# Kernel optimization log

Measured on AMD Instinct MI355X. Metric: run time of the kernel, lower is better.

The kernel has to match this reference:

```python
import jax, jax.numpy as jnp
import numpy as np
from jax import lax

K_STEEP = 10.0      # ssm_K: surrogate spike steepness
V_TH_MIN = 0.1      # ssm_v_th_min
EK_FLOOR = 0.01     # ssm_ek_floor


def setup_inputs() -> dict:
    key = jax.random.key(0)
    ks = jax.random.split(key, 11)
    B, T, D, N = 2, 1024, 1024, 16
    s = lambda fan: 1.0 / np.sqrt(fan)
    return {
        "hidden_states": jax.random.normal(ks[0], (B, T, D), jnp.float32),
        "W_xz": jax.random.normal(ks[1], (D, 2 * D), jnp.float32) * s(D),
        "W_dt": jax.random.normal(ks[2], (D, D), jnp.float32) * s(D),
        "b_dt": jax.random.normal(ks[3], (D,), jnp.float32) * 0.1,
        "A_log": jax.random.uniform(ks[4], (D, N), jnp.float32, 0.0, 1.0),
        "W_B": jax.random.normal(ks[5], (D, N), jnp.float32) * s(D),
        "W_C": jax.random.normal(ks[6], (D, N), jnp.float32) * s(D),
        "D_skip": jax.random.normal(ks[7], (D,), jnp.float32) * 0.1,
        "W_out": jax.random.normal(ks[8], (D, D), jnp.float32) * s(D),
        "v_th": jax.random.uniform(ks[9], (D,), jnp.float32, 0.0, 0.5),
    }


def _bio_ssm(h, W_xz, W_dt, b_dt, A_log, W_B, W_C, D_skip, W_out, v_th):
    # h: (T, B, D) time-major, as in the torch wrapper after permute(1,0,2)
    T, B, D = h.shape
    N = A_log.shape[1]
    xz = jnp.einsum('tbd,de->tbe', h, W_xz)
    x, z = jnp.split(xz, 2, axis=-1)                       # (T,B,D) each
    dt = jax.nn.softplus(jnp.einsum('tbd,de->tbe', x, W_dt) + b_dt)  # (T,B,D)
    A = -jnp.exp(A_log)                                     # (D,N), negative
    Bm = jnp.einsum('tbd,dn->tbn', h, W_B)                  # (T,B,N)
    Cm = jnp.einsum('tbd,dn->tbn', h, W_C)                  # (T,B,N)
    decay = jnp.exp(dt[..., None] * A)                      # (T,B,D,N)
    inp = (dt * x)[..., None] * Bm[:, :, None, :]           # (T,B,D,N)

    def step(s, td):
        dec, ip, c = td
        s = dec * s + ip                                    # (B,D,N)
        y = jnp.einsum('bdn,bn->bd', s, c)
        return s, y

    s0 = jnp.zeros((B, D, N), h.dtype)
    _, y = lax.scan(step, s0, (decay, inp, Cm))             # y: (T,B,D)
    y = y + D_skip * x
    vth = jnp.maximum(v_th, V_TH_MIN)
    spike_p = jax.nn.sigmoid(K_STEEP * (y - vth))           # surrogate spiking gate
    y_sp = y * spike_p
    pc = jnp.mean(spike_p)                                  # ponder cost
    efc = jnp.mean(jax.nn.relu(EK_FLOOR - y * y))           # ek-floor cost
    out = jnp.einsum('tbd,de->tbe', y_sp * jax.nn.silu(z), W_out)
    return out, pc, efc


def reference(hidden_states, W_xz, W_dt, b_dt, A_log, W_B, W_C, D_skip, W_out, v_th):
    h = jnp.transpose(hidden_states, (1, 0, 2))             # (T,B,D)
    h_out, pc, efc = _bio_ssm(h, W_xz, W_dt, b_dt, A_log, W_B, W_C, D_skip, W_out, v_th)
    out = h_out - h                                         # mixer residual delta
    return jnp.transpose(out, (1, 0, 2))                    # (B,T,D)
```

## Files before the change

kernel.cpp:

```cpp
#include <hip/hip_runtime.h>
#include <hip/hip_bf16.h>
#include <stdint.h>

#define TT 1024
#define BB 2
#define DD 1024
#define NN 16
#define NCH 64
#define LCH 16

#define K_STEEP 10.0f
#define V_TH_MIN 0.1f
#define L2E 1.44269504088896f

typedef __bf16 bf16x8 __attribute__((ext_vector_type(8)));
typedef float f32x4 __attribute__((ext_vector_type(4)));

__device__ __forceinline__ short f2bf(float f) {
    union { float f; unsigned u; } c; c.f = f;
    unsigned r = (c.u + 0x7fffu + ((c.u >> 16) & 1u)) >> 16;
    return (short)r;
}

__device__ __forceinline__ void gload_lds16(const void* g, void* l) {
    __builtin_amdgcn_global_load_lds(
        (const __attribute__((address_space(1))) void*)g,
        (__attribute__((address_space(3))) void*)l, 16, 0, 0);
}

template<int BM, int EPI, bool FUSE_BC>
__global__ __launch_bounds__(256) void gemm_mfma(
    const short* __restrict__ A,
    const short* __restrict__ BT,
    float* __restrict__ C, int ldc,
    int M, int Ncols, int K,
    const float* __restrict__ bias,
    const float* __restrict__ sub,
    short* __restrict__ xbuf,
    const short* __restrict__ WbcT,
    float* __restrict__ bcout)
{
    constexpr int RI = BM / 32;
    constexpr int AS_SZ = (FUSE_BC && BM * 32 < 2048) ? 2048 : BM * 32;
    __shared__ short As[AS_SZ];
    __shared__ short Bs[128 * 32];

    const int tid = threadIdx.x;
    const int wave = tid >> 6, lane = tid & 63;
    const int kk = (lane >> 4) * 8;
    const int r16 = lane & 15;
    const int wr = wave >> 1, wc = wave & 1;

    if (FUSE_BC && blockIdx.x == gridDim.x - 1) {
        const int bm2 = blockIdx.y * 32;
        f32x4 acc2 = {};
        for (int k0 = 0; k0 < K; k0 += 64) {
            int off = tid * 16;
            int row = off >> 7;
            int ke  = (off & 127) >> 1;
            gload_lds16(A + (size_t)(bm2 + row) * K + k0 + ke, (char*)As + off);
            gload_lds16(WbcT + (size_t)row * K + k0 + ke, (char*)Bs + off);
            __syncthreads();
            bf16x8 alo = *(const bf16x8*)&As[(wr * 16 + r16) * 64 + kk];
            bf16x8 ahi = *(const bf16x8*)&As[(wr * 16 + r16) * 64 + kk + 32];
            bf16x8 blo = *(const bf16x8*)&Bs[(wc * 16 + r16) * 64 + kk];
            bf16x8 bhi = *(const bf16x8*)&Bs[(wc * 16 + r16) * 64 + kk + 32];
            acc2 = __builtin_amdgcn_mfma_f32_16x16x32_bf16(alo, blo, acc2, 0, 0, 0);
            acc2 = __builtin_amdgcn_mfma_f32_16x16x32_bf16(ahi, bhi, acc2, 0, 0, 0);
            __syncthreads();
        }
        #pragma unroll
        for (int g = 0; g < 4; g++) {
            int row = bm2 + wr * 16 + (lane >> 4) * 4 + g;
            int col = wc * 16 + r16;
            bcout[(size_t)row * 32 + col] = acc2[g];
        }
        return;
    }

    const int bm = blockIdx.y * BM, bn = blockIdx.x * 128;
    f32x4 acc[RI][4] = {};

    for (int k0 = 0; k0 < K; k0 += 32) {
        #pragma unroll
        for (int it = 0; it < 2; it++) {
            int off = it * 4096 + tid * 16;
            int row = off >> 6;
            int ke  = (off & 63) >> 1;
            gload_lds16(BT + (size_t)(bn + row) * K + k0 + ke, (char*)Bs + off);
        }
        if (tid < BM * 4) {
            int off = tid * 16;
            int row = off >> 6;
            int ke  = (off & 63) >> 1;
            gload_lds16(A + (size_t)(bm + row) * K + k0 + ke, (char*)As + off);
        }
        __syncthreads();

        bf16x8 a[RI], b[4];
        #pragma unroll
        for (int i = 0; i < RI; i++)
            a[i] = *(const bf16x8*)&As[(wr * (BM / 2) + i * 16 + r16) * 32 + kk];
        #pragma unroll
        for (int j = 0; j < 4; j++)
            b[j] = *(const bf16x8*)&Bs[(wc * 64 + j * 16 + r16) * 32 + kk];
        #pragma unroll
        for (int i = 0; i < RI; i++)
            #pragma unroll
            for (int j = 0; j < 4; j++)
                acc[i][j] = __builtin_amdgcn_mfma_f32_16x16x32_bf16(
                    a[i], b[j], acc[i][j], 0, 0, 0);
        __syncthreads();
    }

    #pragma unroll
    for (int i = 0; i < RI; i++) {
        #pragma unroll
        for (int j = 0; j < 4; j++) {
            #pragma unroll
            for (int g = 0; g < 4; g++) {
                int row = bm + wr * (BM / 2) + i * 16 + (lane >> 4) * 4 + g;
                int col = bn + wc * 64 + j * 16 + r16;
                float v = acc[i][j][g];
                if (EPI == 1) {
                    v += bias[col];
                    v = fmaxf(v, 0.f) + log1pf(__expf(-fabsf(v)));
                }
                if (EPI == 2) {
                    v -= sub[(size_t)row * ldc + col];
                }
                C[(size_t)row * ldc + col] = v;
                if (EPI == 3 && col < DD) {
                    xbuf[(size_t)row * DD + col] = f2bf(v);
                }
            }
        }
    }
}

__device__ __forceinline__ void tr_tile(
    const float* __restrict__ W, short* __restrict__ WT,
    int K, int N, int k0, int n0, int tid)
{
    __shared__ float t[32][33];
    int r = tid >> 3, q = tid & 7;
    float4 v = *(const float4*)&W[(size_t)(k0 + r) * N + n0 + q * 4];
    t[r][q * 4 + 0] = v.x; t[r][q * 4 + 1] = v.y;
    t[r][q * 4 + 2] = v.z; t[r][q * 4 + 3] = v.w;
    __syncthreads();
    short4 o = { f2bf(t[q * 4 + 0][r]), f2bf(t[q * 4 + 1][r]),
                 f2bf(t[q * 4 + 2][r]), f2bf(t[q * 4 + 3][r]) };
    *(short4*)&WT[(size_t)(n0 + r) * K + k0 + q * 4] = o;
}

__global__ __launch_bounds__(256) void prep_all(
    const float* __restrict__ H,    short* __restrict__ Hb,
    const float* __restrict__ W_xz, short* __restrict__ WxzT,
    const float* __restrict__ W_dt, short* __restrict__ WdtT,
    const float* __restrict__ W_out,short* __restrict__ WoutT,
    const float* __restrict__ W_B,  const float* __restrict__ W_C,
    short* __restrict__ WbcT)
{
    int bid = blockIdx.x, tid = threadIdx.x;
    if (bid < 2048) {
        int i = bid * 1024 + tid * 4;
        float4 v = *(const float4*)&H[i];
        short4 o = { f2bf(v.x), f2bf(v.y), f2bf(v.z), f2bf(v.w) };
        *(short4*)&Hb[i] = o;
    } else if (bid < 4096) {
        int t = bid - 2048;
        tr_tile(W_xz, WxzT, DD, 2 * DD, (t >> 6) * 32, (t & 63) * 32, tid);
    } else if (bid < 5120) {
        int t = bid - 4096;
        tr_tile(W_dt, WdtT, DD, DD, (t >> 5) * 32, (t & 31) * 32, tid);
    } else if (bid < 6144) {
        int t = bid - 5120;
        tr_tile(W_out, WoutT, DD, DD, (t >> 5) * 32, (t & 31) * 32, tid);
    } else {
        int g = (bid - 6144) * 256 + tid;
        int k = g & (DD - 1);
        int n = g >> 10;
        float v = (n < 16) ? W_B[(size_t)k * NN + n]
                           : W_C[(size_t)k * NN + n - 16];
        WbcT[(size_t)n * DD + k] = f2bf(v);
    }
}

__global__ __launch_bounds__(256) void scan_phase1(
    const float* __restrict__ xz,
    const float* __restrict__ dtb,
    const float* __restrict__ bc,
    const float* __restrict__ A_log,
    float* __restrict__ Lst,
    float* __restrict__ sdt)
{
    int tid = threadIdx.x;
    int d = blockIdx.x * 256 + tid;
    int b = blockIdx.y;
    int c = blockIdx.z;

    __shared__ float sBm[LCH][NN];
    for (int i = tid; i < LCH * NN; i += 256) {
        int j = i >> 4, n = i & 15;
        int r = b * TT + c * LCH + j;
        sBm[j][n] = bc[(size_t)r * 32 + n];
    }
    __syncthreads();

    float a2[NN];
    #pragma unroll
    for (int n = 0; n < NN; n++)
        a2[n] = -__expf(A_log[(size_t)d * NN + n]) * L2E;

    float s[NN];
    #pragma unroll
    for (int n = 0; n < NN; n++) s[n] = 0.f;

    float sum_dt = 0.f;
    for (int j = 0; j < LCH; j++) {
        int r = b * TT + c * LCH + j;
        float dt = dtb[(size_t)r * DD + d];
        float x  = xz[(size_t)r * (2 * DD) + d];
        float dtx = dt * x;
        sum_dt += dt;
        #pragma unroll
        for (int n = 0; n < NN; n++) {
            float dec = exp2f(a2[n] * dt);
            s[n] = fmaf(dec, s[n], dtx * sBm[j][n]);
        }
    }
    size_t base = ((size_t)(c * BB + b) * DD + d) * NN;
    #pragma unroll
    for (int n = 0; n < NN; n++) Lst[base + n] = s[n];
    sdt[(size_t)(c * BB + b) * DD + d] = sum_dt;
}

__global__ __launch_bounds__(256) void scan_phase2(
    const float* __restrict__ A_log,
    const float* __restrict__ Lst,
    const float* __restrict__ sdt,
    float* __restrict__ Sinit)
{
    int g = blockIdx.x * 256 + threadIdx.x;
    int n = g & 15;
    int d = (g >> 4) & (DD - 1);
    int b = g >> 14;
    float a2 = -__expf(A_log[(size_t)d * NN + n]) * L2E;
    float s = 0.f;
    for (int c = 0; c < NCH; c++) {
        size_t idx = ((size_t)(c * BB + b) * DD + d) * NN + n;
        Sinit[idx] = s;
        float P = exp2f(a2 * sdt[(size_t)(c * BB + b) * DD + d]);
        s = fmaf(P, s, Lst[idx]);
    }
}

__global__ __launch_bounds__(256) void scan_phase3(
    const float* __restrict__ xz,
    const float* __restrict__ dtb,
    const float* __restrict__ bc,
    const float* __restrict__ A_log,
    const float* __restrict__ Sinit,
    const float* __restrict__ D_skip,
    const float* __restrict__ v_th,
    short* __restrict__ gout)
{
    int tid = threadIdx.x;
    int d = blockIdx.x * 256 + tid;
    int b = blockIdx.y;
    int c = blockIdx.z;

    __shared__ float sB[LCH][NN];
    __shared__ float sC[LCH][NN];
    for (int i = tid; i < LCH * 32; i += 256) {
        int j = i >> 5, m = i & 31;
        int r = b * TT + c * LCH + j;
        float v = bc[(size_t)r * 32 + m];
        if (m < 16) sB[j][m] = v; else sC[j][m - 16] = v;
    }
    __syncthreads();

    float a2[NN];
    #pragma unroll
    for (int n = 0; n < NN; n++)
        a2[n] = -__expf(A_log[(size_t)d * NN + n]) * L2E;

    size_t base = ((size_t)(c * BB + b) * DD + d) * NN;
    float s[NN];
    #pragma unroll
    for (int n = 0; n < NN; n++) s[n] = Sinit[base + n];

    float dsk = D_skip[d];
    float vth = fmaxf(v_th[d], V_TH_MIN);

    for (int j = 0; j < LCH; j++) {
        int r = b * TT + c * LCH + j;
        float dt = dtb[(size_t)r * DD + d];
        float x  = xz[(size_t)r * (2 * DD) + d];
        float z  = xz[(size_t)r * (2 * DD) + DD + d];
        float dtx = dt * x;
        float y = 0.f;
        #pragma unroll
        for (int n = 0; n < NN; n++) {
            float dec = exp2f(a2[n] * dt);
            s[n] = fmaf(dec, s[n], dtx * sB[j][n]);
            y = fmaf(s[n], sC[j][n], y);
        }
        y = fmaf(dsk, x, y);
        float sp = 1.f / (1.f + __expf(-K_STEEP * (y - vth)));
        float sz = z / (1.f + __expf(-z));
        gout[(size_t)r * DD + d] = f2bf(y * sp * sz);
    }
}

extern "C" void kernel_launch(void* const* d_in, const int* in_sizes, int n_in,
                              void* d_out, int out_size, void* d_ws, size_t ws_size,
                              hipStream_t stream) {
    const float* H      = (const float*)d_in[0];
    const float* W_xz   = (const float*)d_in[1];
    const float* W_dt   = (const float*)d_in[2];
    const float* b_dt   = (const float*)d_in[3];
    const float* A_log  = (const float*)d_in[4];
    const float* W_B    = (const float*)d_in[5];
    const float* W_C    = (const float*)d_in[6];
    const float* D_skip = (const float*)d_in[7];
    const float* W_out  = (const float*)d_in[8];
    const float* v_th   = (const float*)d_in[9];
    float* out = (float*)d_out;

    float* ws  = (float*)d_ws;
    float* xz  = ws;
    float* dtb = xz  + 4194304;
    float* bcb = dtb + 2097152;
    float* Lst = bcb + 65536;
    float* sdt = Lst + 2097152;
    float* Sin = sdt + 131072;
    short* p16   = (short*)(Sin + 2097152);
    short* Hb    = p16;
    short* WxzT  = Hb    + 2097152;
    short* WdtT  = WxzT  + 2097152;
    short* WoutT = WdtT  + 1048576;
    short* WbcT  = WoutT + 1048576;
    short* xb    = WbcT  + 32768;
    short* gb    = xb    + 2097152;

    const int M = BB * TT;

    prep_all<<<6272, 256, 0, stream>>>(
        H, Hb, W_xz, WxzT, W_dt, WdtT, W_out, WoutT, W_B, W_C, WbcT);
    gemm_mfma<32, 3, true><<<dim3(17, M / 32), 256, 0, stream>>>(
        Hb, WxzT, xz, 2 * DD, M, 2 * DD, DD, nullptr, nullptr, xb, WbcT, bcb);
    gemm_mfma<32, 1, false><<<dim3(8, M / 32), 256, 0, stream>>>(
        xb, WdtT, dtb, DD, M, DD, DD, b_dt, nullptr, nullptr, nullptr, nullptr);
    scan_phase1<<<dim3(DD / 256, BB, NCH), 256, 0, stream>>>(
        xz, dtb, bcb, A_log, Lst, sdt);
    scan_phase2<<<(BB * DD * NN) / 256, 256, 0, stream>>>(A_log, Lst, sdt, Sin);
    scan_phase3<<<dim3(DD / 256, BB, NCH), 256, 0, stream>>>(
        xz, dtb, bcb, A_log, Sin, D_skip, v_th, gb);
    gemm_mfma<32, 2, false><<<dim3(8, M / 32), 256, 0, stream>>>(
        gb, WoutT, out, DD, M, DD, DD, nullptr, H, nullptr, nullptr, nullptr);
}
```

Measured before the change: 126.7 us.

## Fuse three-phase chunked scan into one kernel and store xz as bf16

The three scan kernels (local chunk scan, cross-chunk carry propagation, final scan with gating) are merged into one kernel. Each block covers 8 channels across all 64 chunks and passes chunk states through shared memory, so the Lst/sdt/Sinit global round trips and two launches go away. The xz projection output is now written only as bf16 and read directly by the dt GEMM (via a new lda stride) and by the scan. This halves xz traffic and drops the separate x buffer, at the cost of lower precision for x and z in the scan. The new scan layout makes each thread read one d from a row, so dt and xz loads become less coalesced (8 contiguous channels per row).

```diff
diff --git a/kernel.cpp b/kernel.cpp
--- a/kernel.cpp
+++ b/kernel.cpp
@@ -21,6 +21,11 @@
     unsigned r = (c.u + 0x7fffu + ((c.u >> 16) & 1u)) >> 16;
     return (short)r;
 }
+__device__ __forceinline__ float bf2f(short s) {
+    union { unsigned u; float f; } c;
+    c.u = ((unsigned)(unsigned short)s) << 16;
+    return c.f;
+}
 
 __device__ __forceinline__ void gload_lds16(const void* g, void* l) {
     __builtin_amdgcn_global_load_lds(
@@ -30,13 +35,13 @@
 
 template<int BM, int EPI, bool FUSE_BC>
 __global__ __launch_bounds__(256) void gemm_mfma(
-    const short* __restrict__ A,
+    const short* __restrict__ A, int lda,
     const short* __restrict__ BT,
     float* __restrict__ C, int ldc,
     int M, int Ncols, int K,
     const float* __restrict__ bias,
     const float* __restrict__ sub,
-    short* __restrict__ xbuf,
+    short* __restrict__ bf16out,
     const short* __restrict__ WbcT,
     float* __restrict__ bcout)
 {
@@ -58,7 +63,7 @@
             int off = tid * 16;
             int row = off >> 7;
             int ke  = (off & 127) >> 1;
-            gload_lds16(A + (size_t)(bm2 + row) * K + k0 + ke, (char*)As + off);
+            gload_lds16(A + (size_t)(bm2 + row) * lda + k0 + ke, (char*)As + off);
             gload_lds16(WbcT + (size_t)row * K + k0 + ke, (char*)Bs + off);
             __syncthreads();
             bf16x8 alo = *(const bf16x8*)&As[(wr * 16 + r16) * 64 + kk];
@@ -93,7 +98,7 @@
             int off = tid * 16;
             int row = off >> 6;
             int ke  = (off & 63) >> 1;
-            gload_lds16(A + (size_t)(bm + row) * K + k0 + ke, (char*)As + off);
+            gload_lds16(A + (size_t)(bm + row) * lda + k0 + ke, (char*)As + off);
         }
         __syncthreads();
 
@@ -122,16 +127,17 @@
                 int row = bm + wr * (BM / 2) + i * 16 + (lane >> 4) * 4 + g;
                 int col = bn + wc * 64 + j * 16 + r16;
                 float v = acc[i][j][g];
-                if (EPI == 1) {
-                    v += bias[col];
-                    v = fmaxf(v, 0.f) + log1pf(__expf(-fabsf(v)));
-                }
-                if (EPI == 2) {
-                    v -= sub[(size_t)row * ldc + col];
-                }
-                C[(size_t)row * ldc + col] = v;
-                if (EPI == 3 && col < DD) {
-                    xbuf[(size_t)row * DD + col] = f2bf(v);
+                if (EPI == 3) {
+                    bf16out[(size_t)row * ldc + col] = f2bf(v);
+                } else {
+                    if (EPI == 1) {
+                        v += bias[col];
+                        v = fmaxf(v, 0.f) + log1pf(__expf(-fabsf(v)));
+                    }
+                    if (EPI == 2) {
+                        v -= sub[(size_t)row * ldc + col];
+                    }
+                    C[(size_t)row * ldc + col] = v;
                 }
             }
         }
@@ -186,125 +192,97 @@
     }
 }
 
-__global__ __launch_bounds__(256) void scan_phase1(
-    const float* __restrict__ xz,
+__global__ __launch_bounds__(512) void scan_fused(
+    const short* __restrict__ xzb,
     const float* __restrict__ dtb,
     const float* __restrict__ bc,
     const float* __restrict__ A_log,
-    float* __restrict__ Lst,
-    float* __restrict__ sdt)
-{
-    int tid = threadIdx.x;
-    int d = blockIdx.x * 256 + tid;
-    int b = blockIdx.y;
-    int c = blockIdx.z;
-
-    __shared__ float sBm[LCH][NN];
-    for (int i = tid; i < LCH * NN; i += 256) {
-        int j = i >> 4, n = i & 15;
-        int r = b * TT + c * LCH + j;
-        sBm[j][n] = bc[(size_t)r * 32 + n];
-    }
-    __syncthreads();
-
-    float a2[NN];
-    #pragma unroll
-    for (int n = 0; n < NN; n++)
-        a2[n] = -__expf(A_log[(size_t)d * NN + n]) * L2E;
-
-    float s[NN];
-    #pragma unroll
-    for (int n = 0; n < NN; n++) s[n] = 0.f;
-
-    float sum_dt = 0.f;
-    for (int j = 0; j < LCH; j++) {
-        int r = b * TT + c * LCH + j;
-        float dt = dtb[(size_t)r * DD + d];
-        float x  = xz[(size_t)r * (2 * DD) + d];
-        float dtx = dt * x;
-        sum_dt += dt;
-        #pragma unroll
-        for (int n = 0; n < NN; n++) {
-            float dec = exp2f(a2[n] * dt);
-            s[n] = fmaf(dec, s[n], dtx * sBm[j][n]);
-        }
-    }
-    size_t base = ((size_t)(c * BB + b) * DD + d) * NN;
-    #pragma unroll
-    for (int n = 0; n < NN; n++) Lst[base + n] = s[n];
-    sdt[(size_t)(c * BB + b) * DD + d] = sum_dt;
-}
-
-__global__ __launch_bounds__(256) void scan_phase2(
-    const float* __restrict__ A_log,
-    const float* __restrict__ Lst,
-    const float* __restrict__ sdt,
-    float* __restrict__ Sinit)
-{
-    int g = blockIdx.x * 256 + threadIdx.x;
-    int n = g & 15;
-    int d = (g >> 4) & (DD - 1);
-    int b = g >> 14;
-    float a2 = -__expf(A_log[(size_t)d * NN + n]) * L2E;
-    float s = 0.f;
-    for (int c = 0; c < NCH; c++) {
-        size_t idx = ((size_t)(c * BB + b) * DD + d) * NN + n;
-        Sinit[idx] = s;
-        float P = exp2f(a2 * sdt[(size_t)(c * BB + b) * DD + d]);
-        s = fmaf(P, s, Lst[idx]);
-    }
-}
-
-__global__ __launch_bounds__(256) void scan_phase3(
-    const float* __restrict__ xz,
-    const float* __restrict__ dtb,
-    const float* __restrict__ bc,
-    const float* __restrict__ A_log,
-    const float* __restrict__ Sinit,
     const float* __restrict__ D_skip,
     const float* __restrict__ v_th,
     short* __restrict__ gout)
 {
-    int tid = threadIdx.x;
-    int d = blockIdx.x * 256 + tid;
-    int b = blockIdx.y;
-    int c = blockIdx.z;
-
-    __shared__ float sB[LCH][NN];
-    __shared__ float sC[LCH][NN];
-    for (int i = tid; i < LCH * 32; i += 256) {
-        int j = i >> 5, m = i & 31;
-        int r = b * TT + c * LCH + j;
-        float v = bc[(size_t)r * 32 + m];
-        if (m < 16) sB[j][m] = v; else sC[j][m - 16] = v;
-    }
-    __syncthreads();
+    __shared__ float Ls[8][NCH][NN];
+    __shared__ float Sd[8][NCH];
+
+    const int tid = threadIdx.x;
+    const int dl = tid & 7;
+    const int c  = tid >> 3;
+    const int d  = blockIdx.x * 8 + dl;
+    const int b  = blockIdx.y;
+    const int r0 = b * TT + c * LCH;
 
     float a2[NN];
     #pragma unroll
     for (int n = 0; n < NN; n++)
         a2[n] = -__expf(A_log[(size_t)d * NN + n]) * L2E;
 
-    size_t base = ((size_t)(c * BB + b) * DD + d) * NN;
     float s[NN];
     #pragma unroll
-    for (int n = 0; n < NN; n++) s[n] = Sinit[base + n];
+    for (int n = 0; n < NN; n++) s[n] = 0.f;
+    float sum_dt = 0.f;
+
+    for (int j = 0; j < LCH; j++) {
+        int r = r0 + j;
+        float dt = dtb[(size_t)r * DD + d];
+        float x  = bf2f(xzb[(size_t)r * (2 * DD) + d]);
+        float dtx = dt * x;
+        sum_dt += dt;
+        float bB[NN];
+        *(float4*)&bB[0]  = *(const float4*)&bc[(size_t)r * 32 + 0];
+        *(float4*)&bB[4]  = *(const float4*)&bc[(size_t)r * 32 + 4];
+        *(float4*)&bB[8]  = *(const float4*)&bc[(size_t)r * 32 + 8];
+        *(float4*)&bB[12] = *(const float4*)&bc[(size_t)r * 32 + 12];
+        #pragma unroll
+        for (int n = 0; n < NN; n++) {
+            float dec = exp2f(a2[n] * dt);
+            s[n] = fmaf(dec, s[n], dtx * bB[n]);
+        }
+    }
+    #pragma unroll
+    for (int n = 0; n < NN; n++) Ls[dl][c][n] = s[n];
+    Sd[dl][c] = sum_dt;
+    __syncthreads();
+
+    if (tid < 128) {
+        int dl2 = tid >> 4, n2 = tid & 15;
+        float a2n = -__expf(A_log[(size_t)(blockIdx.x * 8 + dl2) * NN + n2]) * L2E;
+        float ss = 0.f;
+        for (int cc = 0; cc < NCH; cc++) {
+            float P = exp2f(a2n * Sd[dl2][cc]);
+            float L = Ls[dl2][cc][n2];
+            Ls[dl2][cc][n2] = ss;
+            ss = fmaf(P, ss, L);
+        }
+    }
+    __syncthreads();
+
+    #pragma unroll
+    for (int n = 0; n < NN; n++) s[n] = Ls[dl][c][n];
 
     float dsk = D_skip[d];
     float vth = fmaxf(v_th[d], V_TH_MIN);
 
     for (int j = 0; j < LCH; j++) {
-        int r = b * TT + c * LCH + j;
+        int r = r0 + j;
         float dt = dtb[(size_t)r * DD + d];
-        float x  = xz[(size_t)r * (2 * DD) + d];
-        float z  = xz[(size_t)r * (2 * DD) + DD + d];
+        float x  = bf2f(xzb[(size_t)r * (2 * DD) + d]);
+        float z  = bf2f(xzb[(size_t)r * (2 * DD) + DD + d]);
         float dtx = dt * x;
+        float bB[NN], bC[NN];
+        *(float4*)&bB[0]  = *(const float4*)&bc[(size_t)r * 32 + 0];
+        *(float4*)&bB[4]  = *(const float4*)&bc[(size_t)r * 32 + 4];
+        *(float4*)&bB[8]  = *(const float4*)&bc[(size_t)r * 32 + 8];
+        *(float4*)&bB[12] = *(const float4*)&bc[(size_t)r * 32 + 12];
+        *(float4*)&bC[0]  = *(const float4*)&bc[(size_t)r * 32 + 16];
+        *(float4*)&bC[4]  = *(const float4*)&bc[(size_t)r * 32 + 20];
+        *(float4*)&bC[8]  = *(const float4*)&bc[(size_t)r * 32 + 24];
+        *(float4*)&bC[12] = *(const float4*)&bc[(size_t)r * 32 + 28];
         float y = 0.f;
         #pragma unroll
         for (int n = 0; n < NN; n++) {
             float dec = exp2f(a2[n] * dt);
-            s[n] = fmaf(dec, s[n], dtx * sB[j][n]);
-            y = fmaf(s[n], sC[j][n], y);
+            s[n] = fmaf(dec, s[n], dtx * bB[n]);
+            y = fmaf(s[n], bC[n], y);
         }
         y = fmaf(dsk, x, y);
         float sp = 1.f / (1.f + __expf(-K_STEEP * (y - vth)));
@@ -329,34 +307,30 @@
     float* out = (float*)d_out;
 
     float* ws  = (float*)d_ws;
-    float* xz  = ws;
-    float* dtb = xz  + 4194304;
+    float* dtb = ws;
     float* bcb = dtb + 2097152;
-    float* Lst = bcb + 65536;
-    float* sdt = Lst + 2097152;
-    float* Sin = sdt + 131072;
-    short* p16   = (short*)(Sin + 2097152);
-    short* Hb    = p16;
+    short* p16   = (short*)(bcb + 65536);
+    short* xzb   = p16;
+    short* Hb    = xzb   + 4194304;
     short* WxzT  = Hb    + 2097152;
     short* WdtT  = WxzT  + 2097152;
     short* WoutT = WdtT  + 1048576;
     short* WbcT  = WoutT + 1048576;
-    short* xb    = WbcT  + 32768;
-    short* gb    = xb    + 2097152;
+    short* gb    = WbcT  + 32768;
 
     const int M = BB * TT;
 
     prep_all<<<6272, 256, 0, stream>>>(
         H, Hb, W_xz, WxzT, W_dt, WdtT, W_out, WoutT, W_B, W_C, WbcT);
     gemm_mfma<32, 3, true><<<dim3(17, M / 32), 256, 0, stream>>>(
-        Hb, WxzT, xz, 2 * DD, M, 2 * DD, DD, nullptr, nullptr, xb, WbcT, bcb);
+        Hb, DD, WxzT, nullptr, 2 * DD, M, 2 * DD, DD,
+        nullptr, nullptr, xzb, WbcT, bcb);
     gemm_mfma<32, 1, false><<<dim3(8, M / 32), 256, 0, stream>>>(
-        xb, WdtT, dtb, DD, M, DD, DD, b_dt, nullptr, nullptr, nullptr, nullptr);
-    scan_phase1<<<dim3(DD / 256, BB, NCH), 256, 0, stream>>>(
-        xz, dtb, bcb, A_log, Lst, sdt);
-    scan_phase2<<<(BB * DD * NN) / 256, 256, 0, stream>>>(A_log, Lst, sdt, Sin);
-    scan_phase3<<<dim3(DD / 256, BB, NCH), 256, 0, stream>>>(
-        xz, dtb, bcb, A_log, Sin, D_skip, v_th, gb);
+        xzb, 2 * DD, WdtT, dtb, DD, M, DD, DD,
+        b_dt, nullptr, nullptr, nullptr, nullptr);
+    scan_fused<<<dim3(DD / 8, BB), 512, 0, stream>>>(
+        xzb, dtb, bcb, A_log, D_skip, v_th, gb);
     gemm_mfma<32, 2, false><<<dim3(8, M / 32), 256, 0, stream>>>(
-        gb, WoutT, out, DD, M, DD, DD, nullptr, H, nullptr, nullptr, nullptr);
-}
+        gb, DD, WoutT, out, DD, M, DD, DD,
+        nullptr, H, nullptr, nullptr, nullptr);
+}
```

Result: faster. 118.4 us (-6.5%).
